# Optimization experiments

Hardware: AMD Instinct MI355X
Metric: run time of the kernel (lower is better)

Reference implementation:

```python
import jax, jax.numpy as jnp
import numpy as np

TEMPERATURE = 1.0 / 13.544


def setup_inputs() -> dict:
    key = jax.random.key(0)
    x = jax.random.normal(key, (8, 2048, 128), dtype=jnp.float32)
    return {"x": x, "is_batch_mode": 1}


def reference(x, is_batch_mode):
    # batched pairwise squared-L2 distance via norm expansion:
    # d[b,i,j] = ||x_i||^2 - 2 x_i . x_j + ||x_j||^2
    sq = jnp.sum(x * x, axis=-1)                       # [B, N]
    dots = jnp.einsum('bnd,bmd->bnm', x, x)            # [B, N, N]
    dist = sq[:, :, None] - 2.0 * dots + sq[:, None, :]
    dist = jnp.maximum(dist, 0.0)
    sim = jax.nn.softmax(-TEMPERATURE * dist, axis=-1)  # [B, N, N]
    return sim[..., None]                               # [B, N, N, 1]
```

## Files before the change

kernel.cpp:

```cpp
#include <hip/hip_runtime.h>
#include <hip/hip_bf16.h>
#include <cstdint>


using bf16x8 = __attribute__((ext_vector_type(8))) short;
using f32x4  = __attribute__((ext_vector_type(4))) float;

#define TEMP (1.0f / 13.544f)

#define GLOBAL_AS __attribute__((address_space(1)))
#define LDS_AS    __attribute__((address_space(3)))

__global__ __launch_bounds__(256) void prep_kernel(
    const float* __restrict__ x, uint4* __restrict__ xbf, float* __restrict__ csq)
{
    const int t   = threadIdx.x;
    const int lr  = t >> 4;
    const int q   = t & 15;
    const int row = blockIdx.x * 16 + lr;

    const float* xp = x + (size_t)row * 128 + q * 8;
    float4 a0 = *(const float4*)(xp);
    float4 a1 = *(const float4*)(xp + 4);
    float v[8] = {a0.x, a0.y, a0.z, a0.w, a1.x, a1.y, a1.z, a1.w};

    unsigned u[8];
    float s = 0.f;
#pragma unroll
    for (int e = 0; e < 8; ++e) {
        unsigned ui = __float_as_uint(v[e]);
        unsigned r  = (ui + 0x7FFFu + ((ui >> 16) & 1u)) >> 16;
        u[e] = r;
        float d = __uint_as_float(r << 16);
        s += d * d;
    }
    uint4 pack;
    pack.x = u[0] | (u[1] << 16);
    pack.y = u[2] | (u[3] << 16);
    pack.z = u[4] | (u[5] << 16);
    pack.w = u[6] | (u[7] << 16);

    const int b  = row >> 11;
    const int g  = (row >> 4) & 127;
    const int rr = row & 15;
    xbf[(b * 128 + g) * 256 + q * 16 + rr] = pack;

#pragma unroll
    for (int m = 1; m < 16; m <<= 1) s += __shfl_xor(s, m, 64);
    if (q == 0) csq[row] = s * (-TEMP);
}

__global__ __launch_bounds__(256, 2) void sim_kernel(
    const uint4* __restrict__ xbf, const float* __restrict__ csq, float* __restrict__ out)
{
    const int blk  = blockIdx.x;
    const int b    = blk >> 6;
    const int i0   = (blk & 63) * 32;
    const int tid  = threadIdx.x;
    const int w    = tid >> 6;
    const int lane = tid & 63;
    const int quad = lane >> 4;
    const int l15  = lane & 15;

    __shared__ __align__(16) ushort lsB[16384];
    __shared__ float lsSum[4][32];
    __shared__ float lsInv[32];

    const uint4* xbb  = xbf + (size_t)b * (128 * 256);
    const float* csqb = csq + b * 2048;

    bf16x8 afrag[2][4];
#pragma unroll
    for (int m = 0; m < 2; ++m)
#pragma unroll
        for (int k4 = 0; k4 < 4; ++k4) {
            uint4 vv = xbb[((i0 >> 4) + m) * 256 + (k4 * 4 + quad) * 16 + l15];
            afrag[m][k4] = __builtin_bit_cast(bf16x8, vv);
        }

    float csqi[2][4];
#pragma unroll
    for (int m = 0; m < 2; ++m) {
        float4 vv = *(const float4*)(csqb + i0 + m * 16 + quad * 4);
        csqi[m][0] = vv.x; csqi[m][1] = vv.y; csqi[m][2] = vv.z; csqi[m][3] = vv.w;
    }

    const float C2 = 2.0f * TEMP;
    const int   c0 = w * 32;
    float* outrow = out + ((size_t)b * 2048 + i0) * 2048;

    float sum_[2][4] = {};
    float inv_[2][4];

#pragma unroll 1
    for (int pass = 0; pass < 2; ++pass) {
#pragma unroll 1
        for (int jt = 0; jt < 16; ++jt) {
            const int j0 = jt * 128;
            __syncthreads();
            {
                const uint4* src = xbb + (j0 >> 4) * 256 + w * 512 + lane;
#pragma unroll
                for (int it = 0; it < 8; ++it) {
                    __builtin_amdgcn_global_load_lds(
                        (const GLOBAL_AS void*)(src + it * 64),
                        (LDS_AS void*)(&lsB[w * 4096 + it * 512]),
                        16, 0, 0);
                }
            }
            __syncthreads();

            const float csqj0 = csqb[j0 + c0 + l15];
            const float csqj1 = csqb[j0 + c0 + 16 + l15];

            f32x4 acc[2][2] = {};
#pragma unroll
            for (int k4 = 0; k4 < 4; ++k4) {
                const int qq = k4 * 4 + quad;
                bf16x8 b0 = *(const bf16x8*)(&lsB[(w * 2 + 0) * 2048 + qq * 128 + l15 * 8]);
                bf16x8 b1 = *(const bf16x8*)(&lsB[(w * 2 + 1) * 2048 + qq * 128 + l15 * 8]);
#pragma unroll
                for (int m = 0; m < 2; ++m) {
                    acc[m][0] = __builtin_amdgcn_mfma_f32_16x16x32_bf16(afrag[m][k4], b0, acc[m][0], 0, 0, 0);
                    acc[m][1] = __builtin_amdgcn_mfma_f32_16x16x32_bf16(afrag[m][k4], b1, acc[m][1], 0, 0, 0);
                }
            }

            if (pass == 0) {
#pragma unroll
                for (int m = 0; m < 2; ++m)
#pragma unroll
                    for (int n = 0; n < 2; ++n) {
                        const float cj = n ? csqj1 : csqj0;
#pragma unroll
                        for (int r = 0; r < 4; ++r) {
                            float lg = fminf(fmaf(C2, acc[m][n][r], csqi[m][r] + cj), 0.f);
                            sum_[m][r] += __expf(lg);
                        }
                    }
            } else {
#pragma unroll
                for (int m = 0; m < 2; ++m)
#pragma unroll
                    for (int r = 0; r < 4; ++r) {
                        float* op = outrow + (size_t)(m * 16 + quad * 4 + r) * 2048 + j0 + c0 + l15;
#pragma unroll
                        for (int n = 0; n < 2; ++n) {
                            const float cj = n ? csqj1 : csqj0;
                            float lg = fminf(fmaf(C2, acc[m][n][r], csqi[m][r] + cj), 0.f);
                            op[n * 16] = __expf(lg) * inv_[m][r];
                        }
                    }
            }
        }

        if (pass == 0) {
#pragma unroll
            for (int m = 0; m < 2; ++m)
#pragma unroll
                for (int r = 0; r < 4; ++r) {
                    float s = sum_[m][r];
                    s += __shfl_xor(s, 1, 64);
                    s += __shfl_xor(s, 2, 64);
                    s += __shfl_xor(s, 4, 64);
                    s += __shfl_xor(s, 8, 64);
                    sum_[m][r] = s;
                }
            if (l15 == 0) {
#pragma unroll
                for (int m = 0; m < 2; ++m)
#pragma unroll
                    for (int r = 0; r < 4; ++r)
                        lsSum[w][m * 16 + quad * 4 + r] = sum_[m][r];
            }
            __syncthreads();
            if (tid < 32) {
                float tot = lsSum[0][tid] + lsSum[1][tid] + lsSum[2][tid] + lsSum[3][tid];
                lsInv[tid] = 1.0f / tot;
            }
            __syncthreads();
#pragma unroll
            for (int m = 0; m < 2; ++m) {
                float4 vv = *(const float4*)(&lsInv[m * 16 + quad * 4]);
                inv_[m][0] = vv.x; inv_[m][1] = vv.y; inv_[m][2] = vv.z; inv_[m][3] = vv.w;
            }
        }
    }
}

extern "C" void kernel_launch(void* const* d_in, const int* in_sizes, int n_in,
                              void* d_out, int out_size, void* d_ws, size_t ws_size,
                              hipStream_t stream) {
    const float* x   = (const float*)d_in[0];
    float*       out = (float*)d_out;
    uint4* xbf = (uint4*)d_ws;
    float* csq = (float*)((char*)d_ws + (size_t)4 * 1024 * 1024);

    prep_kernel<<<1024, 256, 0, stream>>>(x, xbf, csq);
    sim_kernel<<<512, 256, 0, stream>>>(xbf, csq, out);
}
```

Measured before the change: 172.7 us.

## Keep softmax numerators in registers to avoid second GEMM pass

Each block now handles 16 rows instead of 32 and keeps all 2048 exponentiated values per row in registers (128 floats per thread), so the second pass that recomputed the MFMA dot products and exponentials is dropped. The grid doubles to 1024 blocks to keep the same total work, and the exponent uses exp2 with log2(e) folded into the precomputed norms and scale. The cost is heavy register pressure, with possible spills or lower occupancy under launch_bounds(256,2), and stores are deferred to the end of the kernel rather than overlapped with compute.

```diff
diff --git a/kernel.cpp b/kernel.cpp
--- a/kernel.cpp
+++ b/kernel.cpp
@@ -6,7 +6,8 @@
 using bf16x8 = __attribute__((ext_vector_type(8))) short;
 using f32x4  = __attribute__((ext_vector_type(4))) float;
 
-#define TEMP (1.0f / 13.544f)
+#define TEMP   (1.0f / 13.544f)
+#define LOG2E  1.4426950408889634f
 
 #define GLOBAL_AS __attribute__((address_space(1)))
 #define LDS_AS    __attribute__((address_space(3)))
@@ -47,15 +48,15 @@
 
 #pragma unroll
     for (int m = 1; m < 16; m <<= 1) s += __shfl_xor(s, m, 64);
-    if (q == 0) csq[row] = s * (-TEMP);
+    if (q == 0) csq[row] = s * (-TEMP * LOG2E);
 }
 
 __global__ __launch_bounds__(256, 2) void sim_kernel(
     const uint4* __restrict__ xbf, const float* __restrict__ csq, float* __restrict__ out)
 {
     const int blk  = blockIdx.x;
-    const int b    = blk >> 6;
-    const int i0   = (blk & 63) * 32;
+    const int b    = blk >> 7;
+    const int i0   = (blk & 127) * 16;
     const int tid  = threadIdx.x;
     const int w    = tid >> 6;
     const int lane = tid & 63;
@@ -63,127 +64,107 @@
     const int l15  = lane & 15;
 
     __shared__ __align__(16) ushort lsB[16384];
-    __shared__ float lsSum[4][32];
-    __shared__ float lsInv[32];
+    __shared__ float lsSum[4][16];
+    __shared__ __align__(16) float lsInv[16];
 
     const uint4* xbb  = xbf + (size_t)b * (128 * 256);
     const float* csqb = csq + b * 2048;
 
-    bf16x8 afrag[2][4];
+    bf16x8 afrag[4];
 #pragma unroll
-    for (int m = 0; m < 2; ++m)
+    for (int k4 = 0; k4 < 4; ++k4) {
+        uint4 vv = xbb[(i0 >> 4) * 256 + (k4 * 4 + quad) * 16 + l15];
+        afrag[k4] = __builtin_bit_cast(bf16x8, vv);
+    }
+
+    float csqi[4];
+    {
+        float4 vv = *(const float4*)(csqb + i0 + quad * 4);
+        csqi[0] = vv.x; csqi[1] = vv.y; csqi[2] = vv.z; csqi[3] = vv.w;
+    }
+
+    const float C2L = 2.0f * TEMP * LOG2E;
+    const int   c0  = w * 32;
+
+    float P[16][2][4];
+    float sum_[4] = {};
+
+#pragma unroll
+    for (int jt = 0; jt < 16; ++jt) {
+        const int j0 = jt * 128;
+        __syncthreads();
+        {
+            const uint4* src = xbb + (j0 >> 4) * 256 + w * 512 + lane;
+#pragma unroll
+            for (int it = 0; it < 8; ++it) {
+                __builtin_amdgcn_global_load_lds(
+                    (const GLOBAL_AS void*)(src + it * 64),
+                    (LDS_AS void*)(&lsB[w * 4096 + it * 512]),
+                    16, 0, 0);
+            }
+        }
+        __syncthreads();
+
+        const float csqj0 = csqb[j0 + c0 + l15];
+        const float csqj1 = csqb[j0 + c0 + 16 + l15];
+
+        f32x4 acc[2] = {};
 #pragma unroll
         for (int k4 = 0; k4 < 4; ++k4) {
-            uint4 vv = xbb[((i0 >> 4) + m) * 256 + (k4 * 4 + quad) * 16 + l15];
-            afrag[m][k4] = __builtin_bit_cast(bf16x8, vv);
+            const int qq = k4 * 4 + quad;
+            bf16x8 b0 = *(const bf16x8*)(&lsB[(w * 2 + 0) * 2048 + qq * 128 + l15 * 8]);
+            bf16x8 b1 = *(const bf16x8*)(&lsB[(w * 2 + 1) * 2048 + qq * 128 + l15 * 8]);
+            acc[0] = __builtin_amdgcn_mfma_f32_16x16x32_bf16(afrag[k4], b0, acc[0], 0, 0, 0);
+            acc[1] = __builtin_amdgcn_mfma_f32_16x16x32_bf16(afrag[k4], b1, acc[1], 0, 0, 0);
         }
 
-    float csqi[2][4];
 #pragma unroll
-    for (int m = 0; m < 2; ++m) {
-        float4 vv = *(const float4*)(csqb + i0 + m * 16 + quad * 4);
-        csqi[m][0] = vv.x; csqi[m][1] = vv.y; csqi[m][2] = vv.z; csqi[m][3] = vv.w;
+        for (int n = 0; n < 2; ++n) {
+            const float cj = n ? csqj1 : csqj0;
+#pragma unroll
+            for (int r = 0; r < 4; ++r) {
+                float lg = fminf(fmaf(C2L, acc[n][r], csqi[r] + cj), 0.f);
+                float p  = exp2f(lg);
+                P[jt][n][r] = p;
+                sum_[r] += p;
+            }
+        }
     }
 
-    const float C2 = 2.0f * TEMP;
-    const int   c0 = w * 32;
+#pragma unroll
+    for (int r = 0; r < 4; ++r) {
+        float s = sum_[r];
+        s += __shfl_xor(s, 1, 64);
+        s += __shfl_xor(s, 2, 64);
+        s += __shfl_xor(s, 4, 64);
+        s += __shfl_xor(s, 8, 64);
+        sum_[r] = s;
+    }
+    if (l15 == 0) {
+#pragma unroll
+        for (int r = 0; r < 4; ++r) lsSum[w][quad * 4 + r] = sum_[r];
+    }
+    __syncthreads();
+    if (tid < 16) {
+        float tot = lsSum[0][tid] + lsSum[1][tid] + lsSum[2][tid] + lsSum[3][tid];
+        lsInv[tid] = 1.0f / tot;
+    }
+    __syncthreads();
+
+    float inv_[4];
+    {
+        float4 vv = *(const float4*)(&lsInv[quad * 4]);
+        inv_[0] = vv.x; inv_[1] = vv.y; inv_[2] = vv.z; inv_[3] = vv.w;
+    }
+
     float* outrow = out + ((size_t)b * 2048 + i0) * 2048;
-
-    float sum_[2][4] = {};
-    float inv_[2][4];
-
-#pragma unroll 1
-    for (int pass = 0; pass < 2; ++pass) {
-#pragma unroll 1
-        for (int jt = 0; jt < 16; ++jt) {
-            const int j0 = jt * 128;
-            __syncthreads();
-            {
-                const uint4* src = xbb + (j0 >> 4) * 256 + w * 512 + lane;
 #pragma unroll
-                for (int it = 0; it < 8; ++it) {
-                    __builtin_amdgcn_global_load_lds(
-                        (const GLOBAL_AS void*)(src + it * 64),
-                        (LDS_AS void*)(&lsB[w * 4096 + it * 512]),
-                        16, 0, 0);
-                }
-            }
-            __syncthreads();
-
-            const float csqj0 = csqb[j0 + c0 + l15];
-            const float csqj1 = csqb[j0 + c0 + 16 + l15];
-
-            f32x4 acc[2][2] = {};
+    for (int jt = 0; jt < 16; ++jt) {
 #pragma unroll
-            for (int k4 = 0; k4 < 4; ++k4) {
-                const int qq = k4 * 4 + quad;
-                bf16x8 b0 = *(const bf16x8*)(&lsB[(w * 2 + 0) * 2048 + qq * 128 + l15 * 8]);
-                bf16x8 b1 = *(const bf16x8*)(&lsB[(w * 2 + 1) * 2048 + qq * 128 + l15 * 8]);
-#pragma unroll
-                for (int m = 0; m < 2; ++m) {
-                    acc[m][0] = __builtin_amdgcn_mfma_f32_16x16x32_bf16(afrag[m][k4], b0, acc[m][0], 0, 0, 0);
-                    acc[m][1] = __builtin_amdgcn_mfma_f32_16x16x32_bf16(afrag[m][k4], b1, acc[m][1], 0, 0, 0);
-                }
-            }
-
-            if (pass == 0) {
-#pragma unroll
-                for (int m = 0; m < 2; ++m)
-#pragma unroll
-                    for (int n = 0; n < 2; ++n) {
-                        const float cj = n ? csqj1 : csqj0;
-#pragma unroll
-                        for (int r = 0; r < 4; ++r) {
-                            float lg = fminf(fmaf(C2, acc[m][n][r], csqi[m][r] + cj), 0.f);
-                            sum_[m][r] += __expf(lg);
-                        }
-                    }
-            } else {
-#pragma unroll
-                for (int m = 0; m < 2; ++m)
-#pragma unroll
-                    for (int r = 0; r < 4; ++r) {
-                        float* op = outrow + (size_t)(m * 16 + quad * 4 + r) * 2048 + j0 + c0 + l15;
-#pragma unroll
-                        for (int n = 0; n < 2; ++n) {
-                            const float cj = n ? csqj1 : csqj0;
-                            float lg = fminf(fmaf(C2, acc[m][n][r], csqi[m][r] + cj), 0.f);
-                            op[n * 16] = __expf(lg) * inv_[m][r];
-                        }
-                    }
-            }
-        }
-
-        if (pass == 0) {
-#pragma unroll
-            for (int m = 0; m < 2; ++m)
-#pragma unroll
-                for (int r = 0; r < 4; ++r) {
-                    float s = sum_[m][r];
-                    s += __shfl_xor(s, 1, 64);
-                    s += __shfl_xor(s, 2, 64);
-                    s += __shfl_xor(s, 4, 64);
-                    s += __shfl_xor(s, 8, 64);
-                    sum_[m][r] = s;
-                }
-            if (l15 == 0) {
-#pragma unroll
-                for (int m = 0; m < 2; ++m)
-#pragma unroll
-                    for (int r = 0; r < 4; ++r)
-                        lsSum[w][m * 16 + quad * 4 + r] = sum_[m][r];
-            }
-            __syncthreads();
-            if (tid < 32) {
-                float tot = lsSum[0][tid] + lsSum[1][tid] + lsSum[2][tid] + lsSum[3][tid];
-                lsInv[tid] = 1.0f / tot;
-            }
-            __syncthreads();
-#pragma unroll
-            for (int m = 0; m < 2; ++m) {
-                float4 vv = *(const float4*)(&lsInv[m * 16 + quad * 4]);
-                inv_[m][0] = vv.x; inv_[m][1] = vv.y; inv_[m][2] = vv.z; inv_[m][3] = vv.w;
-            }
+        for (int r = 0; r < 4; ++r) {
+            float* op = outrow + (size_t)(quad * 4 + r) * 2048 + jt * 128 + c0 + l15;
+            op[0]  = P[jt][0][r] * inv_[r];
+            op[16] = P[jt][1][r] * inv_[r];
         }
     }
 }
@@ -197,5 +178,5 @@
     float* csq = (float*)((char*)d_ws + (size_t)4 * 1024 * 1024);
 
     prep_kernel<<<1024, 256, 0, stream>>>(x, xbf, csq);
-    sim_kernel<<<512, 256, 0, stream>>>(xbf, csq, out);
+    sim_kernel<<<1024, 256, 0, stream>>>(xbf, csq, out);
 }
```

Result: no change. 170.2 us (-1.4%).
